# Optimization experiments

Measured on AMD Instinct MI355X. Metric: run time of the kernel, lower is better.

The kernel has to match this reference:

```python
import jax, jax.numpy as jnp
import numpy as np

VOCAB = 10000
HID = 256

def setup_inputs() -> dict:
    key = jax.random.key(0)
    ks = jax.random.split(key, 7)
    B, T = 64, 64
    input_data = jax.random.randint(ks[0], (B, T), 0, VOCAB, dtype=jnp.int32)
    targets = jax.random.randint(ks[1], (B, T), 0, VOCAB, dtype=jnp.int32)
    # Xavier-ish scaled params
    E = jax.random.normal(ks[2], (VOCAB, HID), dtype=jnp.float32) * (1.0 / np.sqrt(HID))
    W_lstm = jax.random.normal(ks[3], (2 * HID, 4 * HID), dtype=jnp.float32) * (1.0 / np.sqrt(2 * HID))
    b_lstm = jnp.zeros((4 * HID,), dtype=jnp.float32)
    W_dense = jax.random.normal(ks[4], (HID, VOCAB), dtype=jnp.float32) * (1.0 / np.sqrt(HID))
    b_dense = jnp.zeros((VOCAB,), dtype=jnp.float32)
    return {"input_data": input_data, "targets": targets, "E": E,
            "W_lstm": W_lstm, "b_lstm": b_lstm, "W_dense": W_dense, "b_dense": b_dense}

def lstm_scan(xs, W, b, h0, c0):
    # xs: [T, B, H] time-major. TF LSTMCell: gates = [x,h]@W + b, order i,j,f,o, forget_bias=1.0
    def step(carry, x):
        h, c = carry
        gates = jnp.concatenate([x, h], axis=-1) @ W + b  # [B, 4H]
        i, j, f, o = jnp.split(gates, 4, axis=-1)
        c_new = jax.nn.sigmoid(f + 1.0) * c + jax.nn.sigmoid(i) * jnp.tanh(j)
        h_new = jax.nn.sigmoid(o) * jnp.tanh(c_new)
        return (h_new, c_new), h_new
    (hT, cT), hs = jax.lax.scan(step, (h0, c0), xs)
    return hs, (hT, cT)

def reference(input_data, targets, E, W_lstm, b_lstm, W_dense, b_dense):
    B, T = input_data.shape
    inputs = E[input_data]                       # [B, T, H] embedding lookup (no dropout: eval)
    xs = jnp.transpose(inputs, (1, 0, 2))        # [T, B, H]
    h0 = jnp.zeros((B, HID), dtype=E.dtype)
    c0 = jnp.zeros((B, HID), dtype=E.dtype)
    hs, _ = lstm_scan(xs, W_lstm, b_lstm, h0, c0)  # [T, B, H]
    outputs = jnp.transpose(hs, (1, 0, 2))       # [B, T, H]
    logits = outputs @ W_dense + b_dense         # [B, T, V]
    logp = jax.nn.log_softmax(logits, axis=-1)
    ce = -jnp.take_along_axis(logp, targets[..., None].astype(jnp.int32), axis=-1)[..., 0]  # [B, T]
    perplexity = jnp.exp(ce)                     # elementwise, as in add_loss_op
    return perplexity
```

## Files before the change

### kernel.cpp

```cpp
#include <hip/hip_runtime.h>
#include <math.h>

#define VOCABN 10000
#define HIDN   256
#define GATES  1024
#define BN     64
#define TN     64
#define BT     4096
#define NCT    625

typedef unsigned int       u32;
typedef unsigned short     u16;
typedef unsigned long long u64;
typedef float v4f __attribute__((ext_vector_type(4)));
typedef short v8s __attribute__((ext_vector_type(8)));

__device__ __forceinline__ float bf2f(u16 u) {
    return __uint_as_float(((u32)u) << 16);
}
__device__ __forceinline__ u16 f2bf(float f) {
    u32 u = __float_as_uint(f);
    u += 0x7FFFu + ((u >> 16) & 1u);
    return (u16)(u >> 16);
}
__device__ __forceinline__ float fast_sigmoid(float x) {
    return 1.0f / (1.0f + __expf(-x));
}
__device__ __forceinline__ float fast_tanh(float x) {
    float e = __expf(-2.0f * fabsf(x));
    float t = (1.0f - e) / (1.0f + e);
    return copysignf(t, x);
}

__global__ __launch_bounds__(256) void k_wfrag(
    const float* __restrict__ src,
    u16*         __restrict__ dst,
    int ncols)
{
    __shared__ u16 lt[HIDN][16];
    const int c = blockIdx.x;
    const int t = threadIdx.x;
    const float* s = src + (size_t)t * ncols + c * 16;
    #pragma unroll
    for (int j4 = 0; j4 < 4; ++j4) {
        float4 v = *(const float4*)(s + j4 * 4);
        lt[t][j4*4+0] = f2bf(v.x);
        lt[t][j4*4+1] = f2bf(v.y);
        lt[t][j4*4+2] = f2bf(v.z);
        lt[t][j4*4+3] = f2bf(v.w);
    }
    __syncthreads();
    #pragma unroll
    for (int h = 0; h < 2; ++h) {
        int f = t + h * 256;
        int q = f >> 6, l = f & 63;
        int m = l & 15, kb = q * 32 + ((l >> 4) & 3) * 8;
        u32 w[4];
        #pragma unroll
        for (int j = 0; j < 4; ++j)
            w[j] = (u32)lt[kb + 2*j][m] | ((u32)lt[kb + 2*j + 1][m] << 16);
        *(uint4*)(dst + (((size_t)c * 8 + q) * 64 + l) * 8) =
            make_uint4(w[0], w[1], w[2], w[3]);
    }
}

__global__ __launch_bounds__(256) void k_xgates(
    const int*   __restrict__ idx,
    const float* __restrict__ E,
    const u16*   __restrict__ Wxf,
    const float* __restrict__ bl,
    float*       __restrict__ gx)
{
    const int r0   = blockIdx.x * 16;
    const int tid  = threadIdx.x;
    const int w    = tid >> 6, lane = tid & 63;
    const int m    = lane & 15, quad = lane >> 4;

    v8s a[8];
    {
        const float* e = E + (size_t)idx[r0 + m] * HIDN + quad * 8;
        #pragma unroll
        for (int q = 0; q < 8; ++q) {
            float4 x0 = *(const float4*)(e + q * 32);
            float4 x1 = *(const float4*)(e + q * 32 + 4);
            uint4 t4 = make_uint4(
                (u32)f2bf(x0.x) | ((u32)f2bf(x0.y) << 16),
                (u32)f2bf(x0.z) | ((u32)f2bf(x0.w) << 16),
                (u32)f2bf(x1.x) | ((u32)f2bf(x1.y) << 16),
                (u32)f2bf(x1.z) | ((u32)f2bf(x1.w) << 16));
            a[q] = *(v8s*)&t4;
        }
    }

    for (int c = w; c < GATES / 16; c += 4) {
        v4f acc = {0.f, 0.f, 0.f, 0.f};
        #pragma unroll
        for (int q = 0; q < 8; ++q) {
            v8s b = *(const v8s*)(Wxf + (((size_t)c * 8 + q) * 64 + lane) * 8);
            acc = __builtin_amdgcn_mfma_f32_16x16x32_bf16(a[q], b, acc, 0, 0, 0);
        }
        const int col = c * 16 + m;
        const float bv = bl[col];
        #pragma unroll
        for (int r = 0; r < 4; ++r)
            gx[(size_t)(r0 + quad * 4 + r) * GATES + col] = acc[r] + bv;
    }
}

__global__ __launch_bounds__(256) void k_plstm(
    const u16*   __restrict__ Whf,
    const float* __restrict__ gx,
    u16*                      Hx,
    u16*         __restrict__ Hb,
    u32*                      bar)
{
    __shared__ uint4 Wl4[4 * 512];
    __shared__ float gl[4][16][16];

    const int tid  = threadIdx.x;
    const int rg   = blockIdx.x >> 4;
    const int ns   = blockIdx.x & 15;
    const int u0   = ns * 16;
    const int w    = tid >> 6;
    const int lane = tid & 63;
    const int m    = lane & 15, kq = lane >> 4;

    {
        const uint4* src = (const uint4*)Whf;
        #pragma unroll
        for (int i = 0; i < 8; ++i) {
            int e  = tid + i * 256;
            int ct = e >> 9, off = e & 511;
            Wl4[e] = src[(size_t)(ct * 16 + ns) * 512 + off];
        }
    }
    {
        float* g0 = (float*)gl;
        #pragma unroll
        for (int j = 0; j < 4; ++j) g0[tid * 4 + j] = 0.0f;
    }
    __syncthreads();

    const u16* Wl = (const u16*)Wl4;

    const int r = tid >> 4, u = tid & 15;
    const int b = rg * 16 + r;
    const float* gxp = gx + (size_t)b * TN * GATES + u0 + u;
    u16* hbp = Hb + (size_t)b * TN * HIDN + u0 + u;
    const int hxw = b * HIDN + u0 + u;
    const int aoff = (rg * 16 + m) * HIDN + kq * 8;

    float cst = 0.0f;
    float4 gxr;
    gxr.x = gxp[0]; gxr.y = gxp[256]; gxr.z = gxp[512]; gxr.w = gxp[768];

    for (int t = 0; t < TN; ++t) {
        float4 gxn = gxr;
        if (t + 1 < TN) {
            const float* p = gxp + (size_t)(t + 1) * GATES;
            gxn.x = p[0]; gxn.y = p[256]; gxn.z = p[512]; gxn.w = p[768];
        }

        if (t > 0) {
            const u64* hsrc = (const u64*)(Hx + (t & 1) * (BN * HIDN) + aoff);
            v4f acc = {0.f, 0.f, 0.f, 0.f};
            #pragma unroll
            for (int q = 0; q < 8; ++q) {
                union { u64 d[2]; v8s v; } av;
                av.d[0] = __hip_atomic_load(hsrc + q * 8,     __ATOMIC_RELAXED,
                                            __HIP_MEMORY_SCOPE_AGENT);
                av.d[1] = __hip_atomic_load(hsrc + q * 8 + 1, __ATOMIC_RELAXED,
                                            __HIP_MEMORY_SCOPE_AGENT);
                v8s bf = *(const v8s*)(Wl + ((w * 8 + q) * 64 + lane) * 8);
                acc = __builtin_amdgcn_mfma_f32_16x16x32_bf16(av.v, bf, acc, 0, 0, 0);
            }
            #pragma unroll
            for (int rr = 0; rr < 4; ++rr)
                gl[w][kq * 4 + rr][m] = acc[rr];
        }
        __syncthreads();

        {
            float ai = gl[0][r][u] + gxr.x;
            float aj = gl[1][r][u] + gxr.y;
            float af = gl[2][r][u] + gxr.z;
            float ao = gl[3][r][u] + gxr.w;
            float ig = fast_sigmoid(ai);
            float fg = fast_sigmoid(af + 1.0f);
            float og = fast_sigmoid(ao);
            float jt = fast_tanh(aj);
            cst = fg * cst + ig * jt;
            float hn = og * fast_tanh(cst);
            u32 hv = f2bf(hn);
            hbp[(size_t)t * HIDN] = (u16)hv;

            if (t + 1 < TN) {
                u32 p1 = __shfl_down(hv, 1);
                u32 p2 = __shfl_down(hv, 2);
                u32 p3 = __shfl_down(hv, 3);
                if ((tid & 3) == 0) {
                    u64 pk = (u64)(hv | (p1 << 16))
                           | ((u64)(p2 | (p3 << 16)) << 32);
                    u64* dst = (u64*)(Hx + (((t & 1) ^ 1) * (BN * HIDN)) + hxw);
                    __hip_atomic_store(dst, pk, __ATOMIC_RELAXED,
                                       __HIP_MEMORY_SCOPE_AGENT);
                }
            }
        }

        if (t + 1 < TN) {
            __syncthreads();
            if (tid == 0) {
                __hip_atomic_fetch_add(&bar[rg * 64], 1u, __ATOMIC_RELAXED,
                                       __HIP_MEMORY_SCOPE_AGENT);
                u32 tgt = (u32)(t + 1) * 16u;
                while (__hip_atomic_load(&bar[rg * 64], __ATOMIC_RELAXED,
                                         __HIP_MEMORY_SCOPE_AGENT) < tgt)
                    __builtin_amdgcn_s_sleep(1);
            }
            __syncthreads();
        }
        gxr = gxn;
    }
}

__global__ __launch_bounds__(256) void k_dense(
    const u16*   __restrict__ Hb,
    const u16*   __restrict__ Wf,
    const float* __restrict__ bd,
    float*       __restrict__ S)
{
    __shared__ float Sl[32];
    const int rg  = blockIdx.x >> 1, hv = blockIdx.x & 1;
    const int r0  = rg * 32;
    const int tid = threadIdx.x;
    const int w   = tid >> 6, lane = tid & 63;
    const int m   = lane & 15, quad = lane >> 4;

    if (tid < 32) Sl[tid] = 0.0f;

    v8s a[2][8];
    #pragma unroll
    for (int rt = 0; rt < 2; ++rt) {
        const u16* hrow = Hb + (size_t)(r0 + rt * 16 + m) * HIDN + quad * 8;
        #pragma unroll
        for (int q = 0; q < 8; ++q)
            a[rt][q] = *(const v8s*)(hrow + q * 32);
    }
    __syncthreads();

    float s[2][4] = {{0.f,0.f,0.f,0.f},{0.f,0.f,0.f,0.f}};
    const int cbeg = hv ? 313 : 0;
    const int cend = hv ? NCT : 313;
    for (int c = cbeg + w; c < cend; c += 4) {
        v4f acc0 = {0.f,0.f,0.f,0.f};
        v4f acc1 = {0.f,0.f,0.f,0.f};
        #pragma unroll
        for (int q = 0; q < 8; ++q) {
            v8s bq = *(const v8s*)(Wf + (((size_t)c * 8 + q) * 64 + lane) * 8);
            acc0 = __builtin_amdgcn_mfma_f32_16x16x32_bf16(a[0][q], bq, acc0, 0, 0, 0);
            acc1 = __builtin_amdgcn_mfma_f32_16x16x32_bf16(a[1][q], bq, acc1, 0, 0, 0);
        }
        float bv = bd[c * 16 + m];
        #pragma unroll
        for (int r = 0; r < 4; ++r) {
            s[0][r] += __expf(acc0[r] + bv);
            s[1][r] += __expf(acc1[r] + bv);
        }
    }

    #pragma unroll
    for (int rt = 0; rt < 2; ++rt)
        #pragma unroll
        for (int r = 0; r < 4; ++r)
            atomicAdd(&Sl[rt * 16 + quad * 4 + r], s[rt][r]);
    __syncthreads();
    if (tid < 32) S[(size_t)hv * BT + r0 + tid] = Sl[tid];
}

__global__ __launch_bounds__(256) void k_target(
    const u16*   __restrict__ Hb,
    const u16*   __restrict__ Wf,
    const float* __restrict__ bd,
    const int*   __restrict__ tgt,
    float*       __restrict__ tl)
{
    const int tid = threadIdx.x;
    const int row = blockIdx.x * 8 + (tid >> 5);
    const int t   = tid & 31;
    const int q   = t >> 2, lq = t & 3;
    const int v   = tgt[row];
    const int c   = v >> 4, vm = v & 15;
    const int kb  = q * 32 + lq * 8;

    v8s h  = *(const v8s*)(Hb + (size_t)row * HIDN + kb);
    v8s wv = *(const v8s*)(Wf + (((size_t)c * 8 + q) * 64 + lq * 16 + vm) * 8);
    float acc = 0.0f;
    #pragma unroll
    for (int j = 0; j < 8; ++j)
        acc = fmaf(bf2f((u16)h[j]), bf2f((u16)wv[j]), acc);
    #pragma unroll
    for (int off = 16; off >= 1; off >>= 1)
        acc += __shfl_down(acc, off, 32);
    if (t == 0) tl[row] = acc + bd[v];
}

__global__ __launch_bounds__(256) void k_final(
    const float* __restrict__ S,
    const float* __restrict__ tl,
    float*       __restrict__ out)
{
    int i = blockIdx.x * 256 + threadIdx.x;
    out[i] = __expf(__logf(S[i] + S[BT + i]) - tl[i]);
}

extern "C" void kernel_launch(void* const* d_in, const int* in_sizes, int n_in,
                              void* d_out, int out_size, void* d_ws, size_t ws_size,
                              hipStream_t stream) {
    const int*   input   = (const int*)  d_in[0];
    const int*   targets = (const int*)  d_in[1];
    const float* E       = (const float*)d_in[2];
    const float* W_lstm  = (const float*)d_in[3];
    const float* b_lstm  = (const float*)d_in[4];
    const float* W_dense = (const float*)d_in[5];
    const float* b_dense = (const float*)d_in[6];
    float* out = (float*)d_out;

    char* ws = (char*)d_ws;
    float* gx  = (float*)ws;
    u16*   Wf  = (u16*)ws;
    u16*   Hb  = (u16*)(ws + ((size_t)16 << 20));
    u16*   Whf = (u16*)(ws + ((size_t)18 << 20));
    u16*   Wxf = (u16*)(ws + ((size_t)18 << 20) + ((size_t)512 << 10));
    u16*   Hx  = (u16*)(ws + ((size_t)19 << 20));
    float* S   = (float*)(ws + ((size_t)19 << 20) + ((size_t)64 << 10));
    float* tl  = (float*)(ws + ((size_t)19 << 20) + ((size_t)96 << 10));
    u32*   bar = (u32*)  (ws + ((size_t)19 << 20) + ((size_t)112 << 10));

    hipMemsetAsync(bar, 0, 1024, stream);
    k_wfrag <<<64,      256, 0, stream>>>(W_lstm,                      Wxf, GATES);
    k_wfrag <<<64,      256, 0, stream>>>(W_lstm + (size_t)HIDN*GATES, Whf, GATES);
    k_xgates<<<BT / 16, 256, 0, stream>>>(input, E, Wxf, b_lstm, gx);
    k_plstm <<<64,      256, 0, stream>>>(Whf, gx, Hx, Hb, bar);
    k_wfrag <<<NCT,     256, 0, stream>>>(W_dense, Wf, VOCABN);
    k_dense <<<256,     256, 0, stream>>>(Hb, Wf, b_dense, S);
    k_target<<<BT / 8,  256, 0, stream>>>(Hb, Wf, b_dense, targets, tl);
    k_final <<<BT / 256,256, 0, stream>>>(S, tl, out);
}
```

Before: 423.4 us.

## Replace LSTM grid barrier with sentinel-polled per-step hidden buffers

Removes the per-timestep atomic counter barrier. Each step's hidden state now goes into its own slot of a buffer pre-filled with 0xFF, and consumers spin until no sentinel remains in the data they need. Each block now handles 32 hidden units (32 blocks instead of 64), doing two MFMAs per K chunk, and the precomputed input gates are stored as bf16 to halve their traffic. The risks are lower accuracy from bf16 gates, a larger memset of the history buffer, and busy-polling on a global-memory sentinel, which is unsafe if a valid bf16 value ever matches the sentinel pattern.

After: 457.5 us. 1.08x slower.

```diff
diff --git a/kernel.cpp b/kernel.cpp
--- a/kernel.cpp
+++ b/kernel.cpp
@@ -15,6 +15,8 @@
 typedef float v4f __attribute__((ext_vector_type(4)));
 typedef short v8s __attribute__((ext_vector_type(8)));
 
+#define SENT 0xFFFFFFFFFFFFFFFFull
+
 __device__ __forceinline__ float bf2f(u16 u) {
     return __uint_as_float(((u32)u) << 16);
 }
@@ -69,7 +71,7 @@
     const float* __restrict__ E,
     const u16*   __restrict__ Wxf,
     const float* __restrict__ bl,
-    float*       __restrict__ gx)
+    u16*         __restrict__ gxb)
 {
     const int r0   = blockIdx.x * 16;
     const int tid  = threadIdx.x;
@@ -103,24 +105,23 @@
         const float bv = bl[col];
         #pragma unroll
         for (int r = 0; r < 4; ++r)
-            gx[(size_t)(r0 + quad * 4 + r) * GATES + col] = acc[r] + bv;
+            gxb[(size_t)(r0 + quad * 4 + r) * GATES + col] = f2bf(acc[r] + bv);
     }
 }
 
 __global__ __launch_bounds__(256) void k_plstm(
     const u16*   __restrict__ Whf,
-    const float* __restrict__ gx,
+    const u16*   __restrict__ gxb,
     u16*                      Hx,
-    u16*         __restrict__ Hb,
-    u32*                      bar)
-{
-    __shared__ uint4 Wl4[4 * 512];
-    __shared__ float gl[4][16][16];
+    u16*         __restrict__ Hb)
+{
+    __shared__ uint4 Wl4[8 * 512];
+    __shared__ float gl[4][16][33];
 
     const int tid  = threadIdx.x;
-    const int rg   = blockIdx.x >> 4;
-    const int ns   = blockIdx.x & 15;
-    const int u0   = ns * 16;
+    const int rg   = blockIdx.x >> 3;
+    const int ns   = blockIdx.x & 7;
+    const int u0   = ns * 32;
     const int w    = tid >> 6;
     const int lane = tid & 63;
     const int m    = lane & 15, kq = lane >> 4;
@@ -128,99 +129,125 @@
     {
         const uint4* src = (const uint4*)Whf;
         #pragma unroll
-        for (int i = 0; i < 8; ++i) {
+        for (int i = 0; i < 16; ++i) {
             int e  = tid + i * 256;
-            int ct = e >> 9, off = e & 511;
-            Wl4[e] = src[(size_t)(ct * 16 + ns) * 512 + off];
-        }
-    }
-    {
-        float* g0 = (float*)gl;
-        #pragma unroll
-        for (int j = 0; j < 4; ++j) g0[tid * 4 + j] = 0.0f;
-    }
+            int tl = e >> 9, off = e & 511;
+            int ct = (tl >> 1) * 16 + ns * 2 + (tl & 1);
+            Wl4[e] = src[(size_t)ct * 512 + off];
+        }
+    }
+    for (int e = tid; e < 4 * 16 * 33; e += 256) ((float*)gl)[e] = 0.0f;
     __syncthreads();
 
     const u16* Wl = (const u16*)Wl4;
 
     const int r = tid >> 4, u = tid & 15;
     const int b = rg * 16 + r;
-    const float* gxp = gx + (size_t)b * TN * GATES + u0 + u;
-    u16* hbp = Hb + (size_t)b * TN * HIDN + u0 + u;
-    const int hxw = b * HIDN + u0 + u;
-    const int aoff = (rg * 16 + m) * HIDN + kq * 8;
-
-    float cst = 0.0f;
-    float4 gxr;
-    gxr.x = gxp[0]; gxr.y = gxp[256]; gxr.z = gxp[512]; gxr.w = gxp[768];
+    const u16* gxp = gxb + (size_t)b * TN * GATES + u0 + u;
+    u16* hbp  = Hb + (size_t)b * TN * HIDN + u0 + u;
+    const size_t hxw = (size_t)b * HIDN + u0 + u;
+    const size_t arow64 = (size_t)(rg * 16 + m) * (HIDN / 4) + kq * 2;
+
+    float cst0 = 0.0f, cst1 = 0.0f;
+    float gr[8], gn[8];
+    #pragma unroll
+    for (int g = 0; g < 4; ++g) {
+        gr[g]     = bf2f(gxp[g * 256]);
+        gr[g + 4] = bf2f(gxp[g * 256 + 16]);
+    }
 
     for (int t = 0; t < TN; ++t) {
-        float4 gxn = gxr;
         if (t + 1 < TN) {
-            const float* p = gxp + (size_t)(t + 1) * GATES;
-            gxn.x = p[0]; gxn.y = p[256]; gxn.z = p[512]; gxn.w = p[768];
+            const u16* p = gxp + (size_t)(t + 1) * GATES;
+            #pragma unroll
+            for (int g = 0; g < 4; ++g) {
+                gn[g]     = bf2f(p[g * 256]);
+                gn[g + 4] = bf2f(p[g * 256 + 16]);
+            }
         }
 
         if (t > 0) {
-            const u64* hsrc = (const u64*)(Hx + (t & 1) * (BN * HIDN) + aoff);
-            v4f acc = {0.f, 0.f, 0.f, 0.f};
+            const u64* hb64 = (const u64*)(Hx) + (size_t)(t - 1) * (BN * HIDN / 4)
+                              + arow64;
+            u64 d0[8], d1[8];
+            #pragma unroll
+            for (int q = 0; q < 8; ++q) { d0[q] = SENT; d1[q] = SENT; }
+            bool ok = false;
+            while (!ok) {
+                u64 t0[8], t1[8];
+                #pragma unroll
+                for (int q = 0; q < 8; ++q) {
+                    t0[q] = __hip_atomic_load(hb64 + q * 8,     __ATOMIC_RELAXED,
+                                              __HIP_MEMORY_SCOPE_AGENT);
+                    t1[q] = __hip_atomic_load(hb64 + q * 8 + 1, __ATOMIC_RELAXED,
+                                              __HIP_MEMORY_SCOPE_AGENT);
+                }
+                ok = true;
+                #pragma unroll
+                for (int q = 0; q < 8; ++q) {
+                    d0[q] = t0[q]; d1[q] = t1[q];
+                    if (t0[q] == SENT || t1[q] == SENT) ok = false;
+                }
+            }
+            v4f acc0 = {0.f,0.f,0.f,0.f}, acc1 = {0.f,0.f,0.f,0.f};
             #pragma unroll
             for (int q = 0; q < 8; ++q) {
                 union { u64 d[2]; v8s v; } av;
-                av.d[0] = __hip_atomic_load(hsrc + q * 8,     __ATOMIC_RELAXED,
-                                            __HIP_MEMORY_SCOPE_AGENT);
-                av.d[1] = __hip_atomic_load(hsrc + q * 8 + 1, __ATOMIC_RELAXED,
-                                            __HIP_MEMORY_SCOPE_AGENT);
-                v8s bf = *(const v8s*)(Wl + ((w * 8 + q) * 64 + lane) * 8);
-                acc = __builtin_amdgcn_mfma_f32_16x16x32_bf16(av.v, bf, acc, 0, 0, 0);
+                av.d[0] = d0[q]; av.d[1] = d1[q];
+                v8s bf0 = *(const v8s*)(Wl + (((w * 2 + 0) * 8 + q) * 64 + lane) * 8);
+                v8s bf1 = *(const v8s*)(Wl + (((w * 2 + 1) * 8 + q) * 64 + lane) * 8);
+                acc0 = __builtin_amdgcn_mfma_f32_16x16x32_bf16(av.v, bf0, acc0, 0, 0, 0);
+                acc1 = __builtin_amdgcn_mfma_f32_16x16x32_bf16(av.v, bf1, acc1, 0, 0, 0);
             }
             #pragma unroll
-            for (int rr = 0; rr < 4; ++rr)
-                gl[w][kq * 4 + rr][m] = acc[rr];
+            for (int rr = 0; rr < 4; ++rr) {
+                gl[w][kq * 4 + rr][m]      = acc0[rr];
+                gl[w][kq * 4 + rr][16 + m] = acc1[rr];
+            }
         }
         __syncthreads();
 
         {
-            float ai = gl[0][r][u] + gxr.x;
-            float aj = gl[1][r][u] + gxr.y;
-            float af = gl[2][r][u] + gxr.z;
-            float ao = gl[3][r][u] + gxr.w;
-            float ig = fast_sigmoid(ai);
-            float fg = fast_sigmoid(af + 1.0f);
-            float og = fast_sigmoid(ao);
-            float jt = fast_tanh(aj);
-            cst = fg * cst + ig * jt;
-            float hn = og * fast_tanh(cst);
-            u32 hv = f2bf(hn);
-            hbp[(size_t)t * HIDN] = (u16)hv;
+            float ai0 = gl[0][r][u]      + gr[0];
+            float aj0 = gl[1][r][u]      + gr[1];
+            float af0 = gl[2][r][u]      + gr[2];
+            float ao0 = gl[3][r][u]      + gr[3];
+            float ai1 = gl[0][r][u + 16] + gr[4];
+            float aj1 = gl[1][r][u + 16] + gr[5];
+            float af1 = gl[2][r][u + 16] + gr[6];
+            float ao1 = gl[3][r][u + 16] + gr[7];
+
+            float ig0 = fast_sigmoid(ai0), fg0 = fast_sigmoid(af0 + 1.0f);
+            float og0 = fast_sigmoid(ao0), jt0 = fast_tanh(aj0);
+            cst0 = fg0 * cst0 + ig0 * jt0;
+            float hn0 = og0 * fast_tanh(cst0);
+            float ig1 = fast_sigmoid(ai1), fg1 = fast_sigmoid(af1 + 1.0f);
+            float og1 = fast_sigmoid(ao1), jt1 = fast_tanh(aj1);
+            cst1 = fg1 * cst1 + ig1 * jt1;
+            float hn1 = og1 * fast_tanh(cst1);
+
+            u32 h0 = f2bf(hn0), h1 = f2bf(hn1);
 
             if (t + 1 < TN) {
-                u32 p1 = __shfl_down(hv, 1);
-                u32 p2 = __shfl_down(hv, 2);
-                u32 p3 = __shfl_down(hv, 3);
+                u32 a1 = __shfl_down(h0, 1), a2 = __shfl_down(h0, 2), a3 = __shfl_down(h0, 3);
+                u32 b1 = __shfl_down(h1, 1), b2 = __shfl_down(h1, 2), b3 = __shfl_down(h1, 3);
                 if ((tid & 3) == 0) {
-                    u64 pk = (u64)(hv | (p1 << 16))
-                           | ((u64)(p2 | (p3 << 16)) << 32);
-                    u64* dst = (u64*)(Hx + (((t & 1) ^ 1) * (BN * HIDN)) + hxw);
-                    __hip_atomic_store(dst, pk, __ATOMIC_RELAXED,
+                    u64* dst = (u64*)(Hx + (size_t)t * (BN * HIDN) + hxw);
+                    u64 pk0 = (u64)(h0 | (a1 << 16)) | ((u64)(a2 | (a3 << 16)) << 32);
+                    u64 pk1 = (u64)(h1 | (b1 << 16)) | ((u64)(b2 | (b3 << 16)) << 32);
+                    __hip_atomic_store(dst,     pk0, __ATOMIC_RELAXED,
+                                       __HIP_MEMORY_SCOPE_AGENT);
+                    __hip_atomic_store(dst + 4, pk1, __ATOMIC_RELAXED,
                                        __HIP_MEMORY_SCOPE_AGENT);
                 }
             }
-        }
-
-        if (t + 1 < TN) {
-            __syncthreads();
-            if (tid == 0) {
-                __hip_atomic_fetch_add(&bar[rg * 64], 1u, __ATOMIC_RELAXED,
-                                       __HIP_MEMORY_SCOPE_AGENT);
-                u32 tgt = (u32)(t + 1) * 16u;
-                while (__hip_atomic_load(&bar[rg * 64], __ATOMIC_RELAXED,
-                                         __HIP_MEMORY_SCOPE_AGENT) < tgt)
-                    __builtin_amdgcn_s_sleep(1);
-            }
-            __syncthreads();
-        }
-        gxr = gxn;
+            hbp[(size_t)t * HIDN]      = (u16)h0;
+            hbp[(size_t)t * HIDN + 16] = (u16)h1;
+        }
+
+        if (t + 1 < TN) __syncthreads();
+        #pragma unroll
+        for (int g = 0; g < 8; ++g) gr[g] = gn[g];
     }
 }
 
@@ -327,21 +354,20 @@
     float* out = (float*)d_out;
 
     char* ws = (char*)d_ws;
-    float* gx  = (float*)ws;
+    u16*   gxb = (u16*)ws;
     u16*   Wf  = (u16*)ws;
-    u16*   Hb  = (u16*)(ws + ((size_t)16 << 20));
-    u16*   Whf = (u16*)(ws + ((size_t)18 << 20));
-    u16*   Wxf = (u16*)(ws + ((size_t)18 << 20) + ((size_t)512 << 10));
-    u16*   Hx  = (u16*)(ws + ((size_t)19 << 20));
-    float* S   = (float*)(ws + ((size_t)19 << 20) + ((size_t)64 << 10));
-    float* tl  = (float*)(ws + ((size_t)19 << 20) + ((size_t)96 << 10));
-    u32*   bar = (u32*)  (ws + ((size_t)19 << 20) + ((size_t)112 << 10));
-
-    hipMemsetAsync(bar, 0, 1024, stream);
+    u16*   Hb  = (u16*)(ws + ((size_t)8  << 20));
+    u16*   Whf = (u16*)(ws + ((size_t)10 << 20));
+    u16*   Wxf = (u16*)(ws + ((size_t)10 << 20) + ((size_t)512 << 10));
+    u16*   Hx  = (u16*)(ws + ((size_t)11 << 20));
+    float* S   = (float*)(ws + ((size_t)13 << 20));
+    float* tl  = (float*)(ws + ((size_t)13 << 20) + ((size_t)32 << 10));
+
+    hipMemsetAsync(Hx, 0xFF, (size_t)2 << 20, stream);
     k_wfrag <<<64,      256, 0, stream>>>(W_lstm,                      Wxf, GATES);
     k_wfrag <<<64,      256, 0, stream>>>(W_lstm + (size_t)HIDN*GATES, Whf, GATES);
-    k_xgates<<<BT / 16, 256, 0, stream>>>(input, E, Wxf, b_lstm, gx);
-    k_plstm <<<64,      256, 0, stream>>>(Whf, gx, Hx, Hb, bar);
+    k_xgates<<<BT / 16, 256, 0, stream>>>(input, E, Wxf, b_lstm, gxb);
+    k_plstm <<<32,      256, 0, stream>>>(Whf, gxb, Hx, Hb);
     k_wfrag <<<NCT,     256, 0, stream>>>(W_dense, Wf, VOCABN);
     k_dense <<<256,     256, 0, stream>>>(Hb, Wf, b_dense, S);
     k_target<<<BT / 8,  256, 0, stream>>>(Hb, Wf, b_dense, targets, tl);
```
